# Kernel optimization log

Hardware: AMD Instinct MI355X
Metric: run time of the kernel (lower is better)

## Reference

```python
import jax, jax.numpy as jnp
import numpy as np

N_EXPERTS = 8
D_MODEL = 1024
D_FF = 4096
N_TOKENS = 2048
TOP_K = 2


def _init_expert_weight(key, shape):
    # torch init: bound = sqrt(3) * (sqrt(1/3) / sqrt(fan_in)) = 1/sqrt(fan_in), fan_in = shape[1]
    bound = 1.0 / np.sqrt(shape[1])
    return jax.random.uniform(key, shape, jnp.float32, -bound, bound)


def setup_inputs() -> dict:
    key = jax.random.key(0)
    kx, ki, kw, k1, k2, k3 = jax.random.split(key, 6)
    x = jax.random.normal(kx, (N_TOKENS, D_MODEL), jnp.float32)
    expert_indices = jax.random.randint(ki, (N_TOKENS, TOP_K), 0, N_EXPERTS, jnp.int32)
    expert_weights = jax.random.uniform(kw, (N_TOKENS, TOP_K), jnp.float32)
    w1 = _init_expert_weight(k1, (N_EXPERTS, D_MODEL, D_FF))
    w2 = _init_expert_weight(k2, (N_EXPERTS, D_MODEL, D_FF))
    w3 = _init_expert_weight(k3, (N_EXPERTS, D_FF, D_MODEL))
    return {"x": x, "expert_indices": expert_indices, "expert_weights": expert_weights,
            "w1": w1, "w2": w2, "w3": w3}


def reference(x, expert_indices, expert_weights, w1, w2, w3):
    n_tokens, d_model = x.shape
    top_k = expert_indices.shape[1]
    n_experts = w1.shape[0]
    A = n_tokens * top_k  # total assignments; static capacity per expert (no overflow possible)

    flat_e = expert_indices.reshape(-1)            # [A]
    flat_w = expert_weights.reshape(-1)            # [A]
    tok_idx = jnp.repeat(jnp.arange(n_tokens), top_k)  # [A]

    order = jnp.argsort(flat_e, stable=True)
    s_tok = tok_idx[order]
    s_e = flat_e[order]
    s_w = flat_w[order]

    counts = jnp.bincount(flat_e, length=n_experts)            # [E]
    seg_starts = jnp.concatenate([jnp.zeros((1,), counts.dtype), jnp.cumsum(counts)[:-1]])
    pos = jnp.arange(A) - seg_starts[s_e]                       # position within expert segment

    # dispatch: padded per-expert batch [E, A, d]
    padded = jnp.zeros((n_experts, A, d_model), x.dtype).at[s_e, pos].set(x[s_tok])

    gate = jax.nn.silu(jnp.einsum('ecd,edf->ecf', padded, w1))
    value = jnp.einsum('ecd,edf->ecf', padded, w2)
    hidden = gate * value
    expert_out = jnp.einsum('ecf,efd->ecd', hidden, w3)        # [E, A, d]

    # combine: gather per-assignment outputs, weight, scatter-add back to tokens
    y = expert_out[s_e, pos] * s_w[:, None]                    # [A, d]
    out = jnp.zeros((n_tokens, d_model), x.dtype).at[s_tok].add(y)
    return out
```

## Files before the change

### kernel.cpp

```cpp
#include <hip/hip_runtime.h>
#include <stdint.h>

#define N_EXPERTS 8
#define D_MODEL 1024
#define D_FF 4096
#define N_TOKENS 2048
#define ASSN 4096
#define ROWS 4224
#define BK 32

using bfrag = __attribute__((ext_vector_type(8))) short;
using f32x4 = __attribute__((ext_vector_type(4))) float;
typedef unsigned short u16;

__device__ __forceinline__ u16 f2bf(float f) {
  uint32_t u = __builtin_bit_cast(uint32_t, f);
  u += 0x7fffu + ((u >> 16) & 1u);
  return (u16)(u >> 16);
}

__device__ __forceinline__ void gll16(const void* g, void* l) {
  __builtin_amdgcn_global_load_lds(
      (const __attribute__((address_space(1))) void*)g,
      (__attribute__((address_space(3))) void*)l, 16, 0, 0);
}

__global__ void k_setup(const int* __restrict__ eidx, const float* __restrict__ ew,
                        int* __restrict__ rowmap, int* __restrict__ arow,
                        int* __restrict__ counts, int* __restrict__ offs) {
  __shared__ int sc[N_EXPERTS], so[N_EXPERTS];
  int t = threadIdx.x;
  if (t < N_EXPERTS) sc[t] = 0;
  __syncthreads();
  for (int a = t; a < ASSN; a += 256) atomicAdd(&sc[eidx[a]], 1);
  __syncthreads();
  if (t == 0) {
    int run = 0;
    for (int e = 0; e < N_EXPERTS; e++) {
      counts[e] = sc[e]; offs[e] = run; so[e] = run; run += sc[e];
    }
  }
  __syncthreads();
  for (int a = t; a < ASSN; a += 256) {
    int e = eidx[a];
    int p = atomicAdd(&so[e], 1);
    rowmap[p] = a;
    arow[a] = p;
  }
}

__global__ void k_gather(const float* __restrict__ x, const int* __restrict__ rowmap,
                         u16* __restrict__ Xg) {
  int r = blockIdx.x, t = threadIdx.x;
  uint2 o;
  if (r < ASSN) {
    int tok = rowmap[r] >> 1;
    float4 v = *(const float4*)(x + (size_t)tok * D_MODEL + t * 4);
    o.x = (uint32_t)f2bf(v.x) | ((uint32_t)f2bf(v.y) << 16);
    o.y = (uint32_t)f2bf(v.z) | ((uint32_t)f2bf(v.w) << 16);
  } else {
    o.x = 0u; o.y = 0u;
  }
  *(uint2*)(Xg + (size_t)r * D_MODEL + t * 4) = o;
}

__global__ void k_convt(const float* __restrict__ src, u16* __restrict__ dst,
                        int K, int N) {
  const int e = blockIdx.y;
  src += (size_t)e * K * N;
  dst += (size_t)e * K * N;
  const int ntn = N >> 6;
  const int n0 = (blockIdx.x % ntn) << 6;
  const int k0 = (blockIdx.x / ntn) << 7;
  __shared__ u16 T[64][136];
  const int t = threadIdx.x;
  const int rk = t >> 4, rn4 = (t & 15) << 2;
  #pragma unroll
  for (int p = 0; p < 8; p++) {
    const int k = rk + p * 16;
    float4 v = *(const float4*)(src + (size_t)(k0 + k) * N + n0 + rn4);
    T[rn4 + 0][k] = f2bf(v.x);
    T[rn4 + 1][k] = f2bf(v.y);
    T[rn4 + 2][k] = f2bf(v.z);
    T[rn4 + 3][k] = f2bf(v.w);
  }
  __syncthreads();
  const int wn = t >> 4, wk8 = (t & 15) << 3;
  #pragma unroll
  for (int p = 0; p < 4; p++) {
    const int n = wn + p * 16;
    *(bfrag*)(dst + (size_t)(n0 + n) * K + k0 + wk8) = *(const bfrag*)&T[n][wk8];
  }
}

__launch_bounds__(256, 2)
__global__ void k_gemm1(const u16* __restrict__ Xg,
                        const u16* __restrict__ w1t, const u16* __restrict__ w2t,
                        const int* __restrict__ counts, const int* __restrict__ offs,
                        u16* __restrict__ H) {
  const int e = blockIdx.z, nt = blockIdx.x, mt = blockIdx.y;
  const int cnt = counts[e];
  if (mt * 128 >= cnt) return;
  const int row0 = offs[e] + mt * 128;
  const int mrem = cnt - mt * 128;
  const int n0 = nt * 128;

  __shared__ u16 As[2][128 * BK];
  __shared__ u16 B1s[2][128 * BK];
  __shared__ u16 B2s[2][128 * BK];

  const int tid = threadIdx.x;
  const int lane = tid & 63, wave = tid >> 6;
  const int wm = (wave >> 1) << 6, wn = (wave & 1) << 6;
  const int l16 = lane & 15, quad = lane >> 4;

  const int srow = wave * 32 + (lane >> 2);
  const int scol = (lane & 3) * 8;
  const int ld0 = wave * 1024;

  const u16* pA  = Xg  + (size_t)(row0 + srow) * D_MODEL + scol;
  const u16* pB1 = w1t + (size_t)e * D_MODEL * D_FF + (size_t)(n0 + srow) * D_MODEL + scol;
  const u16* pB2 = w2t + (size_t)e * D_MODEL * D_FF + (size_t)(n0 + srow) * D_MODEL + scol;
  const size_t rstep = (size_t)16 * D_MODEL;

  f32x4 acc1[4][4] = {};
  f32x4 acc2[4][4] = {};

  gll16(pA,          &As[0][ld0]);
  gll16(pA + rstep,  &As[0][ld0 + 512]);
  gll16(pB1,         &B1s[0][ld0]);
  gll16(pB1 + rstep, &B1s[0][ld0 + 512]);
  gll16(pB2,         &B2s[0][ld0]);
  gll16(pB2 + rstep, &B2s[0][ld0 + 512]);
  pA += BK; pB1 += BK; pB2 += BK;
  __syncthreads();

  #pragma unroll 2
  for (int ks = 0; ks < 32; ks++) {
    const int c = ks & 1;
    if (ks < 31) {
      gll16(pA,          &As[1 - c][ld0]);
      gll16(pA + rstep,  &As[1 - c][ld0 + 512]);
      gll16(pB1,         &B1s[1 - c][ld0]);
      gll16(pB1 + rstep, &B1s[1 - c][ld0 + 512]);
      gll16(pB2,         &B2s[1 - c][ld0]);
      gll16(pB2 + rstep, &B2s[1 - c][ld0 + 512]);
      pA += BK; pB1 += BK; pB2 += BK;
    }
    bfrag b1[4], b2[4];
    #pragma unroll
    for (int j = 0; j < 4; j++) {
      b1[j] = *(const bfrag*)&B1s[c][(wn + j * 16 + l16) * BK + quad * 8];
      b2[j] = *(const bfrag*)&B2s[c][(wn + j * 16 + l16) * BK + quad * 8];
    }
    #pragma unroll
    for (int i = 0; i < 4; i++) {
      bfrag a = *(const bfrag*)&As[c][(wm + i * 16 + l16) * BK + quad * 8];
      #pragma unroll
      for (int j = 0; j < 4; j++) {
        acc1[i][j] = __builtin_amdgcn_mfma_f32_16x16x32_bf16(a, b1[j], acc1[i][j], 0, 0, 0);
        acc2[i][j] = __builtin_amdgcn_mfma_f32_16x16x32_bf16(a, b2[j], acc2[i][j], 0, 0, 0);
      }
    }
    __syncthreads();
  }

  #pragma unroll
  for (int i = 0; i < 4; i++) {
    #pragma unroll
    for (int p = 0; p < 4; p++) {
      const int mloc = wm + i * 16 + quad * 4 + p;
      if (mloc < mrem) {
        u16* dst = H + (size_t)(row0 + mloc) * D_FF + n0 + wn + l16;
        #pragma unroll
        for (int j = 0; j < 4; j++) {
          float g = acc1[i][j][p];
          float vv = acc2[i][j][p];
          float h = g / (1.0f + __expf(-g)) * vv;
          dst[j * 16] = f2bf(h);
        }
      }
    }
  }
}

__launch_bounds__(256, 2)
__global__ void k_gemm2(const u16* __restrict__ H, const u16* __restrict__ w3t,
                        const int* __restrict__ counts, const int* __restrict__ offs,
                        float* __restrict__ Y0, float* __restrict__ Y1) {
  const int e = blockIdx.z >> 1, khalf = blockIdx.z & 1;
  const int nt = blockIdx.x, mt = blockIdx.y;
  const int cnt = counts[e];
  if (mt * 128 >= cnt) return;
  const int row0 = offs[e] + mt * 128;
  const int mrem = cnt - mt * 128;
  const int n0 = nt * 128;
  float* __restrict__ Y = khalf ? Y1 : Y0;

  __shared__ u16 As[2][128 * BK];
  __shared__ u16 Bs[2][128 * BK];

  const int tid = threadIdx.x;
  const int lane = tid & 63, wave = tid >> 6;
  const int wm = (wave >> 1) << 6, wn = (wave & 1) << 6;
  const int l16 = lane & 15, quad = lane >> 4;

  const int srow = wave * 32 + (lane >> 2);
  const int scol = (lane & 3) * 8;
  const int ld0 = wave * 1024;

  const u16* pA = H + (size_t)(row0 + srow) * D_FF + khalf * 2048 + scol;
  const u16* pB = w3t + (size_t)e * D_FF * D_MODEL
                + (size_t)(n0 + srow) * D_FF + khalf * 2048 + scol;
  const size_t rstepA = (size_t)16 * D_FF;

  f32x4 acc[4][4] = {};

  gll16(pA,           &As[0][ld0]);
  gll16(pA + rstepA,  &As[0][ld0 + 512]);
  gll16(pB,           &Bs[0][ld0]);
  gll16(pB + rstepA,  &Bs[0][ld0 + 512]);
  pA += BK; pB += BK;
  __syncthreads();

  #pragma unroll 2
  for (int ks = 0; ks < 64; ks++) {
    const int c = ks & 1;
    if (ks < 63) {
      gll16(pA,          &As[1 - c][ld0]);
      gll16(pA + rstepA, &As[1 - c][ld0 + 512]);
      gll16(pB,          &Bs[1 - c][ld0]);
      gll16(pB + rstepA, &Bs[1 - c][ld0 + 512]);
      pA += BK; pB += BK;
    }
    bfrag b[4];
    #pragma unroll
    for (int j = 0; j < 4; j++)
      b[j] = *(const bfrag*)&Bs[c][(wn + j * 16 + l16) * BK + quad * 8];
    #pragma unroll
    for (int i = 0; i < 4; i++) {
      bfrag a = *(const bfrag*)&As[c][(wm + i * 16 + l16) * BK + quad * 8];
      #pragma unroll
      for (int j = 0; j < 4; j++)
        acc[i][j] = __builtin_amdgcn_mfma_f32_16x16x32_bf16(a, b[j], acc[i][j], 0, 0, 0);
    }
    __syncthreads();
  }

  #pragma unroll
  for (int i = 0; i < 4; i++) {
    #pragma unroll
    for (int p = 0; p < 4; p++) {
      const int mloc = wm + i * 16 + quad * 4 + p;
      if (mloc < mrem) {
        float* dst = Y + (size_t)(row0 + mloc) * D_MODEL + n0 + wn + l16;
        #pragma unroll
        for (int j = 0; j < 4; j++) dst[j * 16] = acc[i][j][p];
      }
    }
  }
}

__global__ void k_combine(const float* __restrict__ Y0, const float* __restrict__ Y1,
                          const int* __restrict__ arow, const float* __restrict__ ew,
                          float* __restrict__ out) {
  const int tk = blockIdx.x;
  const int d = threadIdx.x * 4;
  const int a0 = tk * 2, a1 = tk * 2 + 1;
  const int r0 = arow[a0], r1 = arow[a1];
  const float w0 = ew[a0], w1 = ew[a1];
  const float4 p0 = *(const float4*)(Y0 + (size_t)r0 * D_MODEL + d);
  const float4 q0 = *(const float4*)(Y1 + (size_t)r0 * D_MODEL + d);
  const float4 p1 = *(const float4*)(Y0 + (size_t)r1 * D_MODEL + d);
  const float4 q1 = *(const float4*)(Y1 + (size_t)r1 * D_MODEL + d);
  float4 r;
  r.x = w0 * (p0.x + q0.x) + w1 * (p1.x + q1.x);
  r.y = w0 * (p0.y + q0.y) + w1 * (p1.y + q1.y);
  r.z = w0 * (p0.z + q0.z) + w1 * (p1.z + q1.z);
  r.w = w0 * (p0.w + q0.w) + w1 * (p1.w + q1.w);
  *(float4*)(out + (size_t)tk * D_MODEL + d) = r;
}

extern "C" void kernel_launch(void* const* d_in, const int* in_sizes, int n_in,
                              void* d_out, int out_size, void* d_ws, size_t ws_size,
                              hipStream_t stream) {
  const float* x  = (const float*)d_in[0];
  const int* eidx = (const int*)d_in[1];
  const float* ew = (const float*)d_in[2];
  const float* w1 = (const float*)d_in[3];
  const float* w2 = (const float*)d_in[4];
  const float* w3 = (const float*)d_in[5];
  float* out = (float*)d_out;

  char* ws = (char*)d_ws;
  int*   rowmap = (int*)(ws);
  int*   arow   = (int*)(ws + 16384);
  int*   counts = (int*)(ws + 32768);
  int*   offs   = (int*)(ws + 32768 + 64);
  const size_t D0 = 65536;
  const size_t SZ_XG = (size_t)ROWS * D_MODEL * 2;
  const size_t SZ_HB = (size_t)ROWS * D_FF * 2;
  const size_t SZ_Y  = (size_t)ROWS * D_MODEL * 4;
  const size_t SZ_W  = (size_t)N_EXPERTS * D_MODEL * D_FF * 2;
  u16*   Xg  = (u16*)(ws + D0);
  u16*   Hb  = (u16*)(ws + D0 + SZ_XG);
  float* Y0  = (float*)(ws + D0 + SZ_XG + SZ_HB);
  float* Y1  = (float*)(ws + D0 + SZ_XG + SZ_HB + SZ_Y);
  u16*   wt1 = (u16*)(ws + D0 + SZ_XG + SZ_HB + 2 * SZ_Y);
  u16*   wt2 = wt1 + SZ_W / 2;
  u16*   wt3 = wt1;

  k_setup<<<1, 256, 0, stream>>>(eidx, ew, rowmap, arow, counts, offs);
  k_gather<<<ROWS, 256, 0, stream>>>(x, rowmap, Xg);
  k_convt<<<dim3(512, N_EXPERTS), 256, 0, stream>>>(w1, wt1, D_MODEL, D_FF);
  k_convt<<<dim3(512, N_EXPERTS), 256, 0, stream>>>(w2, wt2, D_MODEL, D_FF);
  k_gemm1<<<dim3(D_FF / 128, 32, N_EXPERTS), 256, 0, stream>>>(Xg, wt1, wt2, counts, offs, Hb);
  k_convt<<<dim3(512, N_EXPERTS), 256, 0, stream>>>(w3, wt3, D_FF, D_MODEL);
  k_gemm2<<<dim3(D_MODEL / 128, 32, N_EXPERTS * 2), 256, 0, stream>>>(Hb, wt3, counts, offs, Y0, Y1);
  k_combine<<<N_TOKENS, 256, 0, stream>>>(Y0, Y1, arow, ew, out);
}
```

Baseline: 622.7 us.

## Rework weight transpose tiling and use explicit waitcnt barriers in GEMM loops

The weight convert-transpose kernel now packs two bf16 values per 32-bit LDS word, uses a padded stride of 33 to avoid bank conflicts, and halves the K tile, which doubles the grid. Each output row is written as two 16-byte stores. In both GEMM kernels, the __syncthreads calls are replaced by explicit s_waitcnt vmcnt/lgkmcnt plus raw s_barrier, with sched_barrier fences. This lets the next tile's async global-to-LDS loads stay in flight while the current tile is computed. The risk is correctness: it depends on the vmcnt counts exactly matching the number of outstanding loads.

```diff
diff --git a/kernel.cpp b/kernel.cpp
--- a/kernel.cpp
+++ b/kernel.cpp
@@ -71,26 +71,29 @@
   dst += (size_t)e * K * N;
   const int ntn = N >> 6;
   const int n0 = (blockIdx.x % ntn) << 6;
-  const int k0 = (blockIdx.x / ntn) << 7;
-  __shared__ u16 T[64][136];
+  const int k0 = (blockIdx.x / ntn) << 6;
+  __shared__ uint32_t T2[64 * 33];
   const int t = threadIdx.x;
-  const int rk = t >> 4, rn4 = (t & 15) << 2;
+  const int i4 = (t & 15) << 2;
+  const int q  = t >> 4;
   #pragma unroll
-  for (int p = 0; p < 8; p++) {
-    const int k = rk + p * 16;
-    float4 v = *(const float4*)(src + (size_t)(k0 + k) * N + n0 + rn4);
-    T[rn4 + 0][k] = f2bf(v.x);
-    T[rn4 + 1][k] = f2bf(v.y);
-    T[rn4 + 2][k] = f2bf(v.z);
-    T[rn4 + 3][k] = f2bf(v.w);
+  for (int p = 0; p < 2; p++) {
+    const int kp = q + (p << 4);
+    const float4 r0 = *(const float4*)(src + (size_t)(k0 + 2 * kp    ) * N + n0 + i4);
+    const float4 r1 = *(const float4*)(src + (size_t)(k0 + 2 * kp + 1) * N + n0 + i4);
+    T2[(i4 + 0) * 33 + kp] = (uint32_t)f2bf(r0.x) | ((uint32_t)f2bf(r1.x) << 16);
+    T2[(i4 + 1) * 33 + kp] = (uint32_t)f2bf(r0.y) | ((uint32_t)f2bf(r1.y) << 16);
+    T2[(i4 + 2) * 33 + kp] = (uint32_t)f2bf(r0.z) | ((uint32_t)f2bf(r1.z) << 16);
+    T2[(i4 + 3) * 33 + kp] = (uint32_t)f2bf(r0.w) | ((uint32_t)f2bf(r1.w) << 16);
   }
   __syncthreads();
-  const int wn = t >> 4, wk8 = (t & 15) << 3;
+  const int n = t >> 2, seg = t & 3;
+  uint32_t w[8];
   #pragma unroll
-  for (int p = 0; p < 4; p++) {
-    const int n = wn + p * 16;
-    *(bfrag*)(dst + (size_t)(n0 + n) * K + k0 + wk8) = *(const bfrag*)&T[n][wk8];
-  }
+  for (int j = 0; j < 8; j++) w[j] = T2[n * 33 + (seg << 3) + j];
+  u16* d = dst + (size_t)(n0 + n) * K + k0 + (seg << 4);
+  *(uint4*)d = *(uint4*)&w[0];
+  *(uint4*)(d + 8) = *(uint4*)&w[4];
 }
 
 __launch_bounds__(256, 2)
@@ -133,7 +136,6 @@
   gll16(pB2,         &B2s[0][ld0]);
   gll16(pB2 + rstep, &B2s[0][ld0 + 512]);
   pA += BK; pB1 += BK; pB2 += BK;
-  __syncthreads();
 
   #pragma unroll 2
   for (int ks = 0; ks < 32; ks++) {
@@ -146,7 +148,14 @@
       gll16(pB2,         &B2s[1 - c][ld0]);
       gll16(pB2 + rstep, &B2s[1 - c][ld0 + 512]);
       pA += BK; pB1 += BK; pB2 += BK;
-    }
+      asm volatile("s_waitcnt vmcnt(6)" ::: "memory");
+    } else {
+      asm volatile("s_waitcnt vmcnt(0)" ::: "memory");
+    }
+    __builtin_amdgcn_sched_barrier(0);
+    __builtin_amdgcn_s_barrier();
+    __builtin_amdgcn_sched_barrier(0);
+
     bfrag b1[4], b2[4];
     #pragma unroll
     for (int j = 0; j < 4; j++) {
@@ -162,7 +171,10 @@
         acc2[i][j] = __builtin_amdgcn_mfma_f32_16x16x32_bf16(a, b2[j], acc2[i][j], 0, 0, 0);
       }
     }
-    __syncthreads();
+    __builtin_amdgcn_sched_barrier(0);
+    asm volatile("s_waitcnt lgkmcnt(0)" ::: "memory");
+    __builtin_amdgcn_s_barrier();
+    __builtin_amdgcn_sched_barrier(0);
   }
 
   #pragma unroll
@@ -221,7 +233,6 @@
   gll16(pB,           &Bs[0][ld0]);
   gll16(pB + rstepA,  &Bs[0][ld0 + 512]);
   pA += BK; pB += BK;
-  __syncthreads();
 
   #pragma unroll 2
   for (int ks = 0; ks < 64; ks++) {
@@ -232,7 +243,14 @@
       gll16(pB,          &Bs[1 - c][ld0]);
       gll16(pB + rstepA, &Bs[1 - c][ld0 + 512]);
       pA += BK; pB += BK;
-    }
+      asm volatile("s_waitcnt vmcnt(4)" ::: "memory");
+    } else {
+      asm volatile("s_waitcnt vmcnt(0)" ::: "memory");
+    }
+    __builtin_amdgcn_sched_barrier(0);
+    __builtin_amdgcn_s_barrier();
+    __builtin_amdgcn_sched_barrier(0);
+
     bfrag b[4];
     #pragma unroll
     for (int j = 0; j < 4; j++)
@@ -244,7 +262,10 @@
       for (int j = 0; j < 4; j++)
         acc[i][j] = __builtin_amdgcn_mfma_f32_16x16x32_bf16(a, b[j], acc[i][j], 0, 0, 0);
     }
-    __syncthreads();
+    __builtin_amdgcn_sched_barrier(0);
+    asm volatile("s_waitcnt lgkmcnt(0)" ::: "memory");
+    __builtin_amdgcn_s_barrier();
+    __builtin_amdgcn_sched_barrier(0);
   }
 
   #pragma unroll
@@ -312,10 +333,10 @@
 
   k_setup<<<1, 256, 0, stream>>>(eidx, ew, rowmap, arow, counts, offs);
   k_gather<<<ROWS, 256, 0, stream>>>(x, rowmap, Xg);
-  k_convt<<<dim3(512, N_EXPERTS), 256, 0, stream>>>(w1, wt1, D_MODEL, D_FF);
-  k_convt<<<dim3(512, N_EXPERTS), 256, 0, stream>>>(w2, wt2, D_MODEL, D_FF);
+  k_convt<<<dim3(1024, N_EXPERTS), 256, 0, stream>>>(w1, wt1, D_MODEL, D_FF);
+  k_convt<<<dim3(1024, N_EXPERTS), 256, 0, stream>>>(w2, wt2, D_MODEL, D_FF);
   k_gemm1<<<dim3(D_FF / 128, 32, N_EXPERTS), 256, 0, stream>>>(Xg, wt1, wt2, counts, offs, Hb);
-  k_convt<<<dim3(512, N_EXPERTS), 256, 0, stream>>>(w3, wt3, D_FF, D_MODEL);
+  k_convt<<<dim3(1024, N_EXPERTS), 256, 0, stream>>>(w3, wt3, D_FF, D_MODEL);
   k_gemm2<<<dim3(D_MODEL / 128, 32, N_EXPERTS * 2), 256, 0, stream>>>(Hb, wt3, counts, offs, Y0, Y1);
   k_combine<<<N_TOKENS, 256, 0, stream>>>(Y0, Y1, arow, ew, out);
 }
```

After: 614.5 us. About the same (-1.3%).
